# Optimization experiments

Hardware: AMD Instinct MI355X
Metric: run time of the kernel (lower is better)

The kernel has to match this reference:

```python
import jax, jax.numpy as jnp
import numpy as np

NUM_HEADS = 16
HIDDEN = 1024
HEAD_DIM = HIDDEN // NUM_HEADS


def setup_inputs() -> dict:
    key = jax.random.key(0)
    ks = jax.random.split(key, 8)
    B, S = 4, 1024
    scale = 0.02
    return {
        "hidden_states": jax.random.normal(ks[0], (B, S, HIDDEN), jnp.float32),
        "attention_mask": jnp.zeros((B, 1, 1, S), jnp.float32),
        "Wq": jax.random.normal(ks[1], (HIDDEN, HIDDEN), jnp.float32) * scale,
        "bq": jnp.zeros((HIDDEN,), jnp.float32),
        "Wk": jax.random.normal(ks[2], (HIDDEN, HIDDEN), jnp.float32) * scale,
        "bk": jnp.zeros((HIDDEN,), jnp.float32),
        "Wv": jax.random.normal(ks[3], (HIDDEN, HIDDEN), jnp.float32) * scale,
        "bv": jnp.zeros((HIDDEN,), jnp.float32),
    }


def _split_heads(x):
    # [B,S,H] -> [B,heads,S,head_dim]
    B, S, _ = x.shape
    return x.reshape(B, S, NUM_HEADS, HEAD_DIM).transpose(0, 2, 1, 3)


def reference(hidden_states, attention_mask, Wq, bq, Wk, bk, Wv, bv):
    # torch.nn.Linear convention: y = x @ W.T + b
    q = _split_heads(hidden_states @ Wq.T + bq)
    k = _split_heads(hidden_states @ Wk.T + bk)
    v = _split_heads(hidden_states @ Wv.T + bv)
    scores = jnp.einsum('bhqd,bhkd->bhqk', q, k) * (HEAD_DIM ** -0.5)
    scores = scores + attention_mask  # broadcast [B,1,1,S]
    probs = jax.nn.softmax(scores, axis=-1)
    context = jnp.einsum('bhqk,bhkd->bhqd', probs, v)  # [B,heads,S,head_dim]
    B, _, S, _ = context.shape
    return context.transpose(0, 2, 1, 3).reshape(B, S, HIDDEN)
```

## Files before the change

### kernel.cpp

```cpp
#include <hip/hip_runtime.h>
#include <hip/hip_bf16.h>
#include <stdint.h>

#define NH 16
#define HID 1024
#define HD 64
#define NB 4
#define SS 1024
#define MTOT (NB*SS)

typedef __attribute__((ext_vector_type(8))) short bf16x8;
typedef __attribute__((ext_vector_type(4))) float f32x4;
typedef __attribute__((ext_vector_type(16))) float f32x16;

#define LOG2E 1.44269504088896f

__device__ __forceinline__ unsigned short f2bf(float f) {
  union { float f; unsigned u; } v; v.f = f;
  unsigned u = v.u;
  return (unsigned short)((u + 0x7FFFu + ((u >> 16) & 1u)) >> 16);
}

__device__ __forceinline__ unsigned cvtpk(float lo, float hi) {
  unsigned r;
  asm("v_cvt_pk_bf16_f32 %0, %1, %2" : "=v"(r) : "v"(lo), "v"(hi));
  return r;
}

__device__ __forceinline__ void pl32swap(unsigned &a, unsigned &b) {
  asm("v_permlane32_swap_b32 %0, %1" : "+v"(a), "+v"(b));
}

__device__ __forceinline__ float exp2fast(float x) {
  float r;
  asm("v_exp_f32 %0, %1" : "=v"(r) : "v"(x));
  return r;
}

__device__ __forceinline__ void async16(void* lds, const void* g) {
  __builtin_amdgcn_global_load_lds(
      (const __attribute__((address_space(1))) unsigned*)g,
      (__attribute__((address_space(3))) unsigned*)lds, 16, 0, 0);
}

__global__ void cvt_all(const float4* __restrict__ X,
                        const float4* __restrict__ Wq,
                        const float4* __restrict__ Wk,
                        const float4* __restrict__ Wv,
                        ushort4* __restrict__ Xb,
                        ushort4* __restrict__ Wb) {
  int i = blockIdx.x * 256 + threadIdx.x;
  const float4* src; ushort4* dst; int idx;
  if (i < (MTOT * HID / 4)) {
    src = X; dst = Xb; idx = i;
  } else {
    int j = i - (MTOT * HID / 4);
    int sel = j >> 18;
    idx = j & 262143;
    src = (sel == 0) ? Wq : (sel == 1) ? Wk : Wv;
    dst = Wb + (size_t)sel * 262144;
  }
  float4 v = src[idx];
  ushort4 o;
  o.x = f2bf(v.x); o.y = f2bf(v.y); o.z = f2bf(v.z); o.w = f2bf(v.w);
  dst[idx] = o;
}

__global__ __launch_bounds__(256) void qkv_gemm(
    const ushort* __restrict__ Xb,
    const ushort* __restrict__ Wb,
    const float* __restrict__ bq,
    const float* __restrict__ bk,
    const float* __restrict__ bv,
    ushort* __restrict__ Q,
    ushort* __restrict__ K,
    ushort* __restrict__ Vt)
{
  __shared__ __attribute__((aligned(16))) ushort Al[3][128 * 32];
  __shared__ __attribute__((aligned(16))) ushort Bl[3][128 * 32];

  int bid = blockIdx.x;
  int swz = (bid & 7) * 96 + (bid >> 3);
  const int nbn = 3072 / 128;
  int bm = swz / nbn, bn = swz % nbn;
  int m0 = bm * 128, n0 = bn * 128;

  int tid = threadIdx.x;
  int wave = tid >> 6, lane = tid & 63;
  int g = lane >> 4, c = lane & 15;
  int wr = wave >> 1, wc = wave & 1;

  int srow = tid >> 2;
  int schunk = tid & 3;
  int ssw = (srow >> 1) & 3;
  const ushort* Asrc0 = Xb + (size_t)(m0 + srow) * 1024 + ((schunk ^ ssw) << 3);
  const ushort* Asrc1 = Xb + (size_t)(m0 + 64 + srow) * 1024 + ((schunk ^ ssw) << 3);
  const ushort* Bsrc0 = Wb + (size_t)(n0 + srow) * 1024 + ((schunk ^ ssw) << 3);
  const ushort* Bsrc1 = Wb + (size_t)(n0 + 64 + srow) * 1024 + ((schunk ^ ssw) << 3);
  int soff = srow * 64 + schunk * 16;

#define GSTAGE(bi) do {                                   \
    char* la_ = (char*)Al[bi]; char* lb_ = (char*)Bl[bi]; \
    async16(la_ + soff,        Asrc0);                    \
    async16(la_ + 4096 + soff, Asrc1);                    \
    async16(lb_ + soff,        Bsrc0);                    \
    async16(lb_ + 4096 + soff, Bsrc1);                    \
    Asrc0 += 32; Asrc1 += 32; Bsrc0 += 32; Bsrc1 += 32;   \
  } while (0)

  f32x4 acc[4][4] = {};
  int rsw = (c >> 1) & 3;
  int ch = ((g ^ rsw) << 4);

  GSTAGE(0);
  GSTAGE(1);

  int cur = 0, nxt = 2;
  for (int ks = 0; ks < 32; ++ks) {
    if (ks < 31) {
      asm volatile("s_waitcnt vmcnt(4)" ::: "memory");
    } else {
      asm volatile("s_waitcnt vmcnt(0)" ::: "memory");
    }
    __builtin_amdgcn_sched_barrier(0);
    __builtin_amdgcn_s_barrier();
    __builtin_amdgcn_sched_barrier(0);
    if (ks < 30) GSTAGE(nxt);

    const char* la = (const char*)Al[cur];
    const char* lb = (const char*)Bl[cur];
    bf16x8 a[4], b[4];
    #pragma unroll
    for (int m = 0; m < 4; ++m)
      a[m] = *(const bf16x8*)(la + (wr * 64 + m * 16 + c) * 64 + ch);
    #pragma unroll
    for (int n = 0; n < 4; ++n)
      b[n] = *(const bf16x8*)(lb + (wc * 64 + n * 16 + c) * 64 + ch);
    __builtin_amdgcn_s_setprio(1);
    #pragma unroll
    for (int m = 0; m < 4; ++m)
      #pragma unroll
      for (int n = 0; n < 4; ++n)
        acc[m][n] = __builtin_amdgcn_mfma_f32_16x16x32_bf16(a[m], b[n], acc[m][n], 0, 0, 0);
    __builtin_amdgcn_s_setprio(0);

    cur = (cur == 2) ? 0 : cur + 1;
    nxt = (nxt == 2) ? 0 : nxt + 1;
  }
#undef GSTAGE

  int sel = n0 >> 10;
  const float* bp = (sel == 0) ? bq : (sel == 1) ? bk : bv;
  float scl = (sel == 0) ? 0.125f * LOG2E : 1.0f;

  #pragma unroll
  for (int n = 0; n < 4; ++n) {
    int nn = (n0 & 1023) + wc * 64 + n * 16 + c;
    float bias = bp[nn];
    int h = nn >> 6, d = nn & 63;
    #pragma unroll
    for (int m = 0; m < 4; ++m) {
      int rowg = m0 + wr * 64 + m * 16 + g * 4;
      int bb = rowg >> 10;
      int s = rowg & 1023;
      #pragma unroll
      for (int r = 0; r < 4; ++r) {
        float val = (acc[m][n][r] + bias) * scl;
        unsigned short ob = f2bf(val);
        if (sel == 0)
          Q[(size_t)((bb * 16 + h) * 1024 + s + r) * 64 + d] = ob;
        else if (sel == 1)
          K[(size_t)((bb * 16 + h) * 1024 + s + r) * 64 + d] = ob;
        else
          Vt[(size_t)((bb * 16 + h) * 64 + d) * 1024 + s + r] = ob;
      }
    }
  }
}

__device__ __forceinline__ void build_pa(const f32x16& p, bf16x8& pa0, bf16x8& pa1) {
  unsigned W0 = cvtpk(p[0],  p[1]);
  unsigned W1 = cvtpk(p[2],  p[3]);
  unsigned W2 = cvtpk(p[4],  p[5]);
  unsigned W3 = cvtpk(p[6],  p[7]);
  unsigned W4 = cvtpk(p[8],  p[9]);
  unsigned W5 = cvtpk(p[10], p[11]);
  unsigned W6 = cvtpk(p[12], p[13]);
  unsigned W7 = cvtpk(p[14], p[15]);
  pl32swap(W0, W2);
  pl32swap(W1, W3);
  pl32swap(W4, W6);
  pl32swap(W5, W7);
  union { unsigned u[4]; bf16x8 v; } a0, a1;
  a0.u[0] = W0; a0.u[1] = W1; a0.u[2] = W2; a0.u[3] = W3;
  a1.u[0] = W4; a1.u[1] = W5; a1.u[2] = W6; a1.u[3] = W7;
  pa0 = a0.v; pa1 = a1.v;
}

__global__ __launch_bounds__(256) void attn(
    const ushort* __restrict__ Q,
    const ushort* __restrict__ K,
    const ushort* __restrict__ Vt,
    const float* __restrict__ mask,
    float* __restrict__ out)
{
  __shared__ __attribute__((aligned(16))) char kv_lds[3][16384];
  __shared__ float mask_s[SS];

  int blk = blockIdx.x;
  int xcd = blk & 7;
  int j = blk >> 3;
  int bh = xcd * 8 + (j >> 3);
  int qt = j & 7;
  int b = bh >> 4, h = bh & 15;
  int tid = threadIdx.x, wave = tid >> 6, lane = tid & 63;
  int r31 = lane & 31, hi = lane >> 5;
  int rsw = r31 & 7;
  int hib = hi << 4;
  int q0 = qt * 128 + wave * 32;

  const ushort* Qb = Q + (size_t)bh * SS * 64;
  const ushort* Kb = K + (size_t)bh * SS * 64;
  const ushort* Vb = Vt + (size_t)bh * 64 * SS;

  for (int i = tid; i < SS; i += 256) mask_s[i] = mask[b * SS + i] * LOG2E;

  bf16x8 qf[4];
  #pragma unroll
  for (int kp = 0; kp < 4; ++kp)
    qf[kp] = *(const bf16x8*)(Qb + (size_t)(q0 + r31) * 64 + kp * 16 + hi * 8);

  int srow = lane >> 3;
  int schunk = lane & 7;
  const ushort* sptr[4];
  int soff[4];
  #pragma unroll
  for (int j2 = 0; j2 < 4; ++j2) {
    soff[j2] = wave * 4096 + j2 * 1024;
    if (wave < 2) {
      int row = wave * 32 + j2 * 8 + srow;
      sptr[j2] = Kb + (size_t)row * 64 + ((schunk ^ srow) << 3);
    } else {
      int d = (wave - 2) * 32 + j2 * 8 + srow;
      sptr[j2] = Vb + (size_t)d * SS + ((schunk ^ srow) << 3);
    }
  }
  const int sstep = (wave < 2) ? 64 * 64 : 64;

#define STAGE(bufidx) do {                              \
    char* lb_ = kv_lds[bufidx];                         \
    async16(lb_ + soff[0], sptr[0]);                    \
    async16(lb_ + soff[1], sptr[1]);                    \
    async16(lb_ + soff[2], sptr[2]);                    \
    async16(lb_ + soff[3], sptr[3]);                    \
    sptr[0] += sstep; sptr[1] += sstep;                 \
    sptr[2] += sstep; sptr[3] += sstep;                 \
  } while (0)

  __syncthreads();
  STAGE(0);
  STAGE(1);

  f32x16 o0 = (f32x16)0.0f, o1 = (f32x16)0.0f;
  float mrow = 0.f, lrow = 0.f;

  int cur = 0, nxt = 2;
  for (int it = 0; it < 16; ++it) {
    if (it < 15) {
      asm volatile("s_waitcnt vmcnt(4)" ::: "memory");
    } else {
      asm volatile("s_waitcnt vmcnt(0)" ::: "memory");
    }
    __builtin_amdgcn_sched_barrier(0);
    __builtin_amdgcn_s_barrier();
    __builtin_amdgcn_sched_barrier(0);
    if (it < 14) STAGE(nxt);

    const char* kb0 = kv_lds[cur];
    const char* vb0 = kv_lds[cur] + 8192;

    f32x16 s0 = (f32x16)0.0f, s1 = (f32x16)0.0f;
    __builtin_amdgcn_s_setprio(1);
    #pragma unroll
    for (int kp = 0; kp < 4; ++kp) {
      int ch = (((kp << 1) | hi) ^ rsw) << 4;
      bf16x8 ka = *(const bf16x8*)(kb0 + r31 * 128 + ch);
      bf16x8 kc = *(const bf16x8*)(kb0 + (32 + r31) * 128 + ch);
      s0 = __builtin_amdgcn_mfma_f32_32x32x16_bf16(ka, qf[kp], s0, 0, 0, 0);
      s1 = __builtin_amdgcn_mfma_f32_32x32x16_bf16(kc, qf[kp], s1, 0, 0, 0);
    }
    __builtin_amdgcn_s_setprio(0);

    int kv = it * 64;
    #pragma unroll
    for (int sq = 0; sq < 4; ++sq) {
      f32x4 mk0 = *(const f32x4*)(&mask_s[kv + sq * 8 + hi * 4]);
      f32x4 mk1 = *(const f32x4*)(&mask_s[kv + 32 + sq * 8 + hi * 4]);
      #pragma unroll
      for (int r = 0; r < 4; ++r) {
        s0[sq * 4 + r] += mk0[r];
        s1[sq * 4 + r] += mk1[r];
      }
    }

    float mx = s0[0];
    #pragma unroll
    for (int i = 1; i < 16; ++i) mx = fmaxf(mx, s0[i]);
    #pragma unroll
    for (int i = 0; i < 16; ++i) mx = fmaxf(mx, s1[i]);
    mx = fmaxf(mx, __shfl_xor(mx, 32));

    if (!__all(mx <= mrow + 11.5416f)) {
      float mn = fmaxf(mrow, mx);
      float sc = exp2fast(mrow - mn);
      mrow = mn;
      lrow *= sc;
      #pragma unroll
      for (int i = 0; i < 16; ++i) {
        int qh = (i & 3) + 8 * (i >> 2);
        float scq = __uint_as_float((unsigned)__builtin_amdgcn_ds_bpermute(
            (qh << 2) + hib, (int)__float_as_uint(sc)));
        o0[i] *= scq; o1[i] *= scq;
      }
    }

    f32x16 p0, p1;
    float rs = 0.f;
    #pragma unroll
    for (int i = 0; i < 16; ++i) { float e = exp2fast(s0[i] - mrow); p0[i] = e; rs += e; }
    #pragma unroll
    for (int i = 0; i < 16; ++i) { float e = exp2fast(s1[i] - mrow); p1[i] = e; rs += e; }
    rs += __shfl_xor(rs, 32);
    lrow += rs;

    #pragma unroll
    for (int T = 0; T < 2; ++T) {
      bf16x8 pa0, pa1;
      build_pa(T ? p1 : p0, pa0, pa1);
      __builtin_amdgcn_s_setprio(1);
      #pragma unroll
      for (int kh = 0; kh < 2; ++kh) {
        int kap = 2 * T + kh;
        int ch = (((kap << 1) | hi) ^ rsw) << 4;
        bf16x8 va = *(const bf16x8*)(vb0 + r31 * 128 + ch);
        bf16x8 vc = *(const bf16x8*)(vb0 + (32 + r31) * 128 + ch);
        bf16x8 pf = kh ? pa1 : pa0;
        o0 = __builtin_amdgcn_mfma_f32_32x32x16_bf16(pf, va, o0, 0, 0, 0);
        o1 = __builtin_amdgcn_mfma_f32_32x32x16_bf16(pf, vc, o1, 0, 0, 0);
      }
      __builtin_amdgcn_s_setprio(0);
    }

    cur = (cur == 2) ? 0 : cur + 1;
    nxt = (nxt == 2) ? 0 : nxt + 1;
  }
#undef STAGE

  float inv = 1.0f / lrow;
  #pragma unroll
  for (int i = 0; i < 16; ++i) {
    int qh = (i & 3) + 8 * (i >> 2);
    float li = __uint_as_float((unsigned)__builtin_amdgcn_ds_bpermute(
        (qh << 2) + hib, (int)__float_as_uint(inv)));
    int row = q0 + qh + 4 * hi;
    float* op = out + (size_t)(b * SS + row) * 1024 + h * 64 + r31;
    op[0]  = o0[i] * li;
    op[32] = o1[i] * li;
  }
}

extern "C" void kernel_launch(void* const* d_in, const int* in_sizes, int n_in,
                              void* d_out, int out_size, void* d_ws, size_t ws_size,
                              hipStream_t stream) {
  const float* hs   = (const float*)d_in[0];
  const float* mask = (const float*)d_in[1];
  const float* Wq   = (const float*)d_in[2];
  const float* bq   = (const float*)d_in[3];
  const float* Wk   = (const float*)d_in[4];
  const float* bk   = (const float*)d_in[5];
  const float* Wv   = (const float*)d_in[6];
  const float* bv   = (const float*)d_in[7];
  float* out = (float*)d_out;

  char* ws = (char*)d_ws;
  ushort* Xb = (ushort*)(ws);
  ushort* Wb = (ushort*)(ws + (8u  << 20));
  ushort* Qp = (ushort*)(ws + (14u << 20));
  ushort* Kp = (ushort*)(ws + (22u << 20));
  ushort* Vt = (ushort*)(ws + (30u << 20));

  cvt_all<<<7168, 256, 0, stream>>>((const float4*)hs, (const float4*)Wq,
                                    (const float4*)Wk, (const float4*)Wv,
                                    (ushort4*)Xb, (ushort4*)Wb);
  qkv_gemm<<<768, 256, 0, stream>>>(Xb, Wb, bq, bk, bv, Qp, Kp, Vt);
  attn<<<512, 256, 0, stream>>>(Qp, Kp, Vt, mask, out);
}
```

Measured before the change: 85.83 us.

## Rewrite QKV GEMM with 256x256 tiles, 8 waves and ping-pong LDS schedule

Replaces the 128x128-tile, 4-wave triple-buffered QKV GEMM with a 256x256-tile, 512-thread kernel. It uses 64-wide K steps, 128KB of double-buffered LDS and an interleaved schedule that alternates sub-tile loads and MFMA groups between barriers. The aim is more data reuse per LDS byte and better overlap of global loads with MFMA. The trade-off is that only 192 blocks are launched, and with 128KB of LDS per block this can leave many CUs idle. The many extra barriers also add sync overhead.

```diff
diff --git a/kernel.cpp b/kernel.cpp
--- a/kernel.cpp
+++ b/kernel.cpp
@@ -66,7 +66,7 @@
   dst[idx] = o;
 }
 
-__global__ __launch_bounds__(256) void qkv_gemm(
+__global__ __launch_bounds__(512, 2) void qkv_gemm(
     const ushort* __restrict__ Xb,
     const ushort* __restrict__ Wb,
     const float* __restrict__ bq,
@@ -76,78 +76,129 @@
     ushort* __restrict__ K,
     ushort* __restrict__ Vt)
 {
-  __shared__ __attribute__((aligned(16))) ushort Al[3][128 * 32];
-  __shared__ __attribute__((aligned(16))) ushort Bl[3][128 * 32];
+  __shared__ __attribute__((aligned(16))) char lds_[131072];
+  char* ldsA = lds_;
+  char* ldsB = lds_ + 65536;
 
   int bid = blockIdx.x;
-  int swz = (bid & 7) * 96 + (bid >> 3);
-  const int nbn = 3072 / 128;
-  int bm = swz / nbn, bn = swz % nbn;
-  int m0 = bm * 128, n0 = bn * 128;
+  int swz = (bid & 7) * 24 + (bid >> 3);
+  int bm = swz / 12, bn = swz % 12;
+  int m0 = bm * 256, n0 = bn * 256;
 
   int tid = threadIdx.x;
   int wave = tid >> 6, lane = tid & 63;
   int g = lane >> 4, c = lane & 15;
-  int wr = wave >> 1, wc = wave & 1;
-
-  int srow = tid >> 2;
-  int schunk = tid & 3;
-  int ssw = (srow >> 1) & 3;
-  const ushort* Asrc0 = Xb + (size_t)(m0 + srow) * 1024 + ((schunk ^ ssw) << 3);
-  const ushort* Asrc1 = Xb + (size_t)(m0 + 64 + srow) * 1024 + ((schunk ^ ssw) << 3);
-  const ushort* Bsrc0 = Wb + (size_t)(n0 + srow) * 1024 + ((schunk ^ ssw) << 3);
-  const ushort* Bsrc1 = Wb + (size_t)(n0 + 64 + srow) * 1024 + ((schunk ^ ssw) << 3);
-  int soff = srow * 64 + schunk * 16;
-
-#define GSTAGE(bi) do {                                   \
-    char* la_ = (char*)Al[bi]; char* lb_ = (char*)Bl[bi]; \
-    async16(la_ + soff,        Asrc0);                    \
-    async16(la_ + 4096 + soff, Asrc1);                    \
-    async16(lb_ + soff,        Bsrc0);                    \
-    async16(lb_ + 4096 + soff, Bsrc1);                    \
-    Asrc0 += 32; Asrc1 += 32; Bsrc0 += 32; Bsrc1 += 32;   \
-  } while (0)
-
-  f32x4 acc[4][4] = {};
-  int rsw = (c >> 1) & 3;
-  int ch = ((g ^ rsw) << 4);
-
-  GSTAGE(0);
-  GSTAGE(1);
-
-  int cur = 0, nxt = 2;
-  for (int ks = 0; ks < 32; ++ks) {
-    if (ks < 31) {
-      asm volatile("s_waitcnt vmcnt(4)" ::: "memory");
-    } else {
-      asm volatile("s_waitcnt vmcnt(0)" ::: "memory");
-    }
-    __builtin_amdgcn_sched_barrier(0);
-    __builtin_amdgcn_s_barrier();
-    __builtin_amdgcn_sched_barrier(0);
-    if (ks < 30) GSTAGE(nxt);
-
-    const char* la = (const char*)Al[cur];
-    const char* lb = (const char*)Bl[cur];
-    bf16x8 a[4], b[4];
-    #pragma unroll
-    for (int m = 0; m < 4; ++m)
-      a[m] = *(const bf16x8*)(la + (wr * 64 + m * 16 + c) * 64 + ch);
-    #pragma unroll
-    for (int n = 0; n < 4; ++n)
-      b[n] = *(const bf16x8*)(lb + (wc * 64 + n * 16 + c) * 64 + ch);
-    __builtin_amdgcn_s_setprio(1);
-    #pragma unroll
-    for (int m = 0; m < 4; ++m)
-      #pragma unroll
-      for (int n = 0; n < 4; ++n)
-        acc[m][n] = __builtin_amdgcn_mfma_f32_16x16x32_bf16(a[m], b[n], acc[m][n], 0, 0, 0);
-    __builtin_amdgcn_s_setprio(0);
-
-    cur = (cur == 2) ? 0 : cur + 1;
-    nxt = (nxt == 2) ? 0 : nxt + 1;
-  }
-#undef GSTAGE
+  int wr = wave >> 2, wc = wave & 3;
+
+  int r0 = tid >> 3, ck = tid & 7;
+  int gck = ck ^ (r0 & 7);
+  const ushort* As0 = Xb + (size_t)(m0 + r0) * 1024 + gck * 8;
+  const ushort* As1 = As0 + 128 * 1024;
+  const ushort* Bs0 = Wb + (size_t)(n0 + r0) * 1024 + gck * 8;
+  const ushort* Bs1 = Bs0 + 128 * 1024;
+  int sdst = tid * 16;
+
+#define STG_A(d, h, t) do { \
+    const ushort* _s = ((h) ? As1 : As0) + (t) * 64; \
+    char* _d = ldsA + ((d) * 2 + (h)) * 16384 + sdst; \
+    async16(_d, _s); async16(_d + 8192, _s + 64 * 1024); } while (0)
+#define STG_B(d, h, t) do { \
+    const ushort* _s = ((h) ? Bs1 : Bs0) + (t) * 64; \
+    char* _d = ldsB + ((d) * 2 + (h)) * 16384 + sdst; \
+    async16(_d, _s); async16(_d + 8192, _s + 64 * 1024); } while (0)
+
+  int ch0 = (g ^ (c & 7)) << 4;
+  int ch1 = ((4 + g) ^ (c & 7)) << 4;
+
+  bf16x8 a[4][2], b[2][2], b2[2][2];
+  f32x4 acc[8][4] = {};
+
+#define LDA_(mlo, d) do { \
+    const char* _p = ldsA + ((d) * 2 + wr) * 16384; \
+    _Pragma("unroll") \
+    for (int mm = 0; mm < 4; ++mm) { \
+      int _ro = ((mlo) * 64 + mm * 16 + c) * 128; \
+      a[mm][0] = *(const bf16x8*)(_p + _ro + ch0); \
+      a[mm][1] = *(const bf16x8*)(_p + _ro + ch1); } } while (0)
+#define LDB_(dst, nlo, d) do { \
+    const char* _p = ldsB + ((d) * 2 + (wc >> 1)) * 16384 + ((wc & 1) * 64) * 128; \
+    _Pragma("unroll") \
+    for (int nn2 = 0; nn2 < 2; ++nn2) { \
+      int _ro = (((nlo) * 2 + nn2) * 16 + c) * 128; \
+      dst[nn2][0] = *(const bf16x8*)(_p + _ro + ch0); \
+      dst[nn2][1] = *(const bf16x8*)(_p + _ro + ch1); } } while (0)
+
+#define BARRIER() do { __builtin_amdgcn_sched_barrier(0); \
+    __builtin_amdgcn_s_barrier(); __builtin_amdgcn_sched_barrier(0); } while (0)
+
+#define MF_(mlo, bf, nlo) do { \
+    __builtin_amdgcn_s_setprio(1); \
+    _Pragma("unroll") \
+    for (int mm = 0; mm < 4; ++mm) \
+      _Pragma("unroll") \
+      for (int nn2 = 0; nn2 < 2; ++nn2) { \
+        acc[(mlo)*4+mm][(nlo)*2+nn2] = __builtin_amdgcn_mfma_f32_16x16x32_bf16( \
+            a[mm][0], bf[nn2][0], acc[(mlo)*4+mm][(nlo)*2+nn2], 0, 0, 0); \
+        acc[(mlo)*4+mm][(nlo)*2+nn2] = __builtin_amdgcn_mfma_f32_16x16x32_bf16( \
+            a[mm][1], bf[nn2][1], acc[(mlo)*4+mm][(nlo)*2+nn2], 0, 0, 0); } \
+    __builtin_amdgcn_s_setprio(0); } while (0)
+
+  STG_B(0, 0, 0); STG_B(0, 1, 0);
+  STG_A(0, 0, 0); STG_A(0, 1, 0);
+  STG_B(1, 0, 1); STG_B(1, 1, 1);
+  asm volatile("s_waitcnt vmcnt(4)" ::: "memory");
+  BARRIER();
+
+  for (int i2 = 0; i2 < 8; ++i2) {
+    int t1 = 2 * i2 + 1, t2 = 2 * i2 + 2, t3 = 2 * i2 + 3;
+    LDA_(0, 0); LDB_(b, 0, 0);
+    STG_A(1, 0, t1);
+    BARRIER();
+    MF_(0, b, 0);
+    BARRIER();
+    LDB_(b2, 1, 0);
+    STG_A(1, 1, t1);
+    BARRIER();
+    MF_(0, b2, 1);
+    BARRIER();
+    LDA_(1, 0);
+    STG_B(0, 0, t2);
+    BARRIER();
+    MF_(1, b, 0);
+    BARRIER();
+    STG_B(0, 1, t2);
+    asm volatile("s_waitcnt vmcnt(4)" ::: "memory");
+    BARRIER();
+    MF_(1, b2, 1);
+    BARRIER();
+    LDA_(0, 1); LDB_(b, 0, 1);
+    STG_A(0, 0, t2);
+    BARRIER();
+    MF_(0, b, 0);
+    BARRIER();
+    LDB_(b2, 1, 1);
+    STG_A(0, 1, t2);
+    BARRIER();
+    MF_(0, b2, 1);
+    BARRIER();
+    LDA_(1, 1);
+    STG_B(1, 0, t3);
+    BARRIER();
+    MF_(1, b, 0);
+    BARRIER();
+    STG_B(1, 1, t3);
+    asm volatile("s_waitcnt vmcnt(4)" ::: "memory");
+    BARRIER();
+    MF_(1, b2, 1);
+    BARRIER();
+  }
+  asm volatile("s_waitcnt vmcnt(0)" ::: "memory");
+#undef STG_A
+#undef STG_B
+#undef LDA_
+#undef LDB_
+#undef MF_
+#undef BARRIER
 
   int sel = n0 >> 10;
   const float* bp = (sel == 0) ? bq : (sel == 1) ? bk : bv;
@@ -159,8 +210,8 @@
     float bias = bp[nn];
     int h = nn >> 6, d = nn & 63;
     #pragma unroll
-    for (int m = 0; m < 4; ++m) {
-      int rowg = m0 + wr * 64 + m * 16 + g * 4;
+    for (int m = 0; m < 8; ++m) {
+      int rowg = m0 + wr * 128 + m * 16 + g * 4;
       int bb = rowg >> 10;
       int s = rowg & 1023;
       #pragma unroll
@@ -392,6 +443,6 @@
   cvt_all<<<7168, 256, 0, stream>>>((const float4*)hs, (const float4*)Wq,
                                     (const float4*)Wk, (const float4*)Wv,
                                     (ushort4*)Xb, (ushort4*)Wb);
-  qkv_gemm<<<768, 256, 0, stream>>>(Xb, Wb, bq, bk, bv, Qp, Kp, Vt);
+  qkv_gemm<<<192, 512, 0, stream>>>(Xb, Wb, bq, bk, bv, Qp, Kp, Vt);
   attn<<<512, 256, 0, stream>>>(Qp, Kp, Vt, mask, out);
 }
```

After: 98.89 us. +15.2%, slower.

## Retile QKV GEMM to 128x64 blocks with two waves and double buffering

Applied to the files above, without the earlier changes.

The QKV projection GEMM moves from 128x128 tiles with four waves and a 3-stage LDS ring to 128x64 tiles with two waves and a 2-stage double buffer, launching twice as many blocks. Each block issues its next-stage loads before waiting and adds a second barrier per k-step to protect buffer reuse. The aim is more blocks in flight across the CUs to fill the machine better on a 768-block grid. In exchange, B-tile reuse per block drops, each wave loads more A data, and pipelining depth shrinks.

```diff
diff --git a/kernel.cpp b/kernel.cpp
--- a/kernel.cpp
+++ b/kernel.cpp
@@ -66,7 +66,7 @@
   dst[idx] = o;
 }
 
-__global__ __launch_bounds__(256) void qkv_gemm(
+__global__ __launch_bounds__(128) void qkv_gemm(
     const ushort* __restrict__ Xb,
     const ushort* __restrict__ Wb,
     const float* __restrict__ bq,
@@ -76,36 +76,41 @@
     ushort* __restrict__ K,
     ushort* __restrict__ Vt)
 {
-  __shared__ __attribute__((aligned(16))) ushort Al[3][128 * 32];
-  __shared__ __attribute__((aligned(16))) ushort Bl[3][128 * 32];
+  __shared__ __attribute__((aligned(16))) ushort Al[2][128 * 32];
+  __shared__ __attribute__((aligned(16))) ushort Bl[2][64 * 32];
 
   int bid = blockIdx.x;
-  int swz = (bid & 7) * 96 + (bid >> 3);
-  const int nbn = 3072 / 128;
-  int bm = swz / nbn, bn = swz % nbn;
-  int m0 = bm * 128, n0 = bn * 128;
+  int swz = (bid & 7) * 192 + (bid >> 3);
+  int bm = swz / 48, bn = swz % 48;
+  int m0 = bm * 128, n0 = bn * 64;
 
   int tid = threadIdx.x;
   int wave = tid >> 6, lane = tid & 63;
   int g = lane >> 4, c = lane & 15;
-  int wr = wave >> 1, wc = wave & 1;
-
-  int srow = tid >> 2;
-  int schunk = tid & 3;
-  int ssw = (srow >> 1) & 3;
-  const ushort* Asrc0 = Xb + (size_t)(m0 + srow) * 1024 + ((schunk ^ ssw) << 3);
-  const ushort* Asrc1 = Xb + (size_t)(m0 + 64 + srow) * 1024 + ((schunk ^ ssw) << 3);
-  const ushort* Bsrc0 = Wb + (size_t)(n0 + srow) * 1024 + ((schunk ^ ssw) << 3);
-  const ushort* Bsrc1 = Wb + (size_t)(n0 + 64 + srow) * 1024 + ((schunk ^ ssw) << 3);
-  int soff = srow * 64 + schunk * 16;
+
+  int r0 = tid >> 2;
+  int ck = tid & 3;
+  int gck = ck ^ ((r0 >> 1) & 3);
+  const ushort* As[4];
+  const ushort* Bs[2];
+  #pragma unroll
+  for (int i = 0; i < 4; ++i)
+    As[i] = Xb + (size_t)(m0 + r0 + 32 * i) * 1024 + gck * 8;
+  #pragma unroll
+  for (int i = 0; i < 2; ++i)
+    Bs[i] = Wb + (size_t)(n0 + r0 + 32 * i) * 1024 + gck * 8;
+  int sdst = tid * 16;
 
 #define GSTAGE(bi) do {                                   \
     char* la_ = (char*)Al[bi]; char* lb_ = (char*)Bl[bi]; \
-    async16(la_ + soff,        Asrc0);                    \
-    async16(la_ + 4096 + soff, Asrc1);                    \
-    async16(lb_ + soff,        Bsrc0);                    \
-    async16(lb_ + 4096 + soff, Bsrc1);                    \
-    Asrc0 += 32; Asrc1 += 32; Bsrc0 += 32; Bsrc1 += 32;   \
+    async16(la_ + sdst,        As[0]);                    \
+    async16(la_ + 2048 + sdst, As[1]);                    \
+    async16(la_ + 4096 + sdst, As[2]);                    \
+    async16(la_ + 6144 + sdst, As[3]);                    \
+    async16(lb_ + sdst,        Bs[0]);                    \
+    async16(lb_ + 2048 + sdst, Bs[1]);                    \
+    As[0] += 32; As[1] += 32; As[2] += 32; As[3] += 32;   \
+    Bs[0] += 32; Bs[1] += 32;                             \
   } while (0)
 
   f32x4 acc[4][4] = {};
@@ -113,29 +118,28 @@
   int ch = ((g ^ rsw) << 4);
 
   GSTAGE(0);
-  GSTAGE(1);
-
-  int cur = 0, nxt = 2;
+
+  int cur = 0;
   for (int ks = 0; ks < 32; ++ks) {
     if (ks < 31) {
-      asm volatile("s_waitcnt vmcnt(4)" ::: "memory");
+      GSTAGE(cur ^ 1);
+      asm volatile("s_waitcnt vmcnt(6)" ::: "memory");
     } else {
       asm volatile("s_waitcnt vmcnt(0)" ::: "memory");
     }
     __builtin_amdgcn_sched_barrier(0);
     __builtin_amdgcn_s_barrier();
     __builtin_amdgcn_sched_barrier(0);
-    if (ks < 30) GSTAGE(nxt);
 
     const char* la = (const char*)Al[cur];
     const char* lb = (const char*)Bl[cur];
     bf16x8 a[4], b[4];
     #pragma unroll
     for (int m = 0; m < 4; ++m)
-      a[m] = *(const bf16x8*)(la + (wr * 64 + m * 16 + c) * 64 + ch);
+      a[m] = *(const bf16x8*)(la + (wave * 64 + m * 16 + c) * 64 + ch);
     #pragma unroll
     for (int n = 0; n < 4; ++n)
-      b[n] = *(const bf16x8*)(lb + (wc * 64 + n * 16 + c) * 64 + ch);
+      b[n] = *(const bf16x8*)(lb + (n * 16 + c) * 64 + ch);
     __builtin_amdgcn_s_setprio(1);
     #pragma unroll
     for (int m = 0; m < 4; ++m)
@@ -144,23 +148,24 @@
         acc[m][n] = __builtin_amdgcn_mfma_f32_16x16x32_bf16(a[m], b[n], acc[m][n], 0, 0, 0);
     __builtin_amdgcn_s_setprio(0);
 
-    cur = (cur == 2) ? 0 : cur + 1;
-    nxt = (nxt == 2) ? 0 : nxt + 1;
+    __builtin_amdgcn_sched_barrier(0);
+    __builtin_amdgcn_s_barrier();
+    cur ^= 1;
   }
 #undef GSTAGE
 
   int sel = n0 >> 10;
   const float* bp = (sel == 0) ? bq : (sel == 1) ? bk : bv;
   float scl = (sel == 0) ? 0.125f * LOG2E : 1.0f;
+  int h = (n0 & 1023) >> 6;
 
   #pragma unroll
   for (int n = 0; n < 4; ++n) {
-    int nn = (n0 & 1023) + wc * 64 + n * 16 + c;
-    float bias = bp[nn];
-    int h = nn >> 6, d = nn & 63;
+    int d = n * 16 + c;
+    float bias = bp[(n0 & 1023) + d];
     #pragma unroll
     for (int m = 0; m < 4; ++m) {
-      int rowg = m0 + wr * 64 + m * 16 + g * 4;
+      int rowg = m0 + wave * 64 + m * 16 + g * 4;
       int bb = rowg >> 10;
       int s = rowg & 1023;
       #pragma unroll
@@ -392,6 +397,6 @@
   cvt_all<<<7168, 256, 0, stream>>>((const float4*)hs, (const float4*)Wq,
                                     (const float4*)Wk, (const float4*)Wv,
                                     (ushort4*)Xb, (ushort4*)Wb);
-  qkv_gemm<<<768, 256, 0, stream>>>(Xb, Wb, bq, bk, bv, Qp, Kp, Vt);
+  qkv_gemm<<<1536, 128, 0, stream>>>(Xb, Wb, bq, bk, bv, Qp, Kp, Vt);
   attn<<<512, 256, 0, stream>>>(Qp, Kp, Vt, mask, out);
 }
```

Result: slower. 93.10 us (+8.5%).

## Load GEMM B and attention V operands directly into registers, bypassing LDS

Applied to the files above, without the earlier changes.

In the QKV GEMM, the W tile is no longer staged through shared memory. Each wave loads its B fragments straight from global memory into double-buffered registers, while X still goes through the LDS ring. The block-to-tile mapping is also changed so each XCD owns a fixed set of M rows, and an occupancy hint is added. In the attention kernel, V fragments are read from global memory into registers each iteration and only K stays in the LDS triple buffer. This cuts LDS use and ds_read traffic, but the direct-to-register global loads are less coalesced and raise register pressure.

```diff
diff --git a/kernel.cpp b/kernel.cpp
--- a/kernel.cpp
+++ b/kernel.cpp
@@ -66,7 +66,7 @@
   dst[idx] = o;
 }
 
-__global__ __launch_bounds__(256) void qkv_gemm(
+__global__ __launch_bounds__(256, 3) void qkv_gemm(
     const ushort* __restrict__ Xb,
     const ushort* __restrict__ Wb,
     const float* __restrict__ bq,
@@ -77,12 +77,12 @@
     ushort* __restrict__ Vt)
 {
   __shared__ __attribute__((aligned(16))) ushort Al[3][128 * 32];
-  __shared__ __attribute__((aligned(16))) ushort Bl[3][128 * 32];
 
   int bid = blockIdx.x;
-  int swz = (bid & 7) * 96 + (bid >> 3);
-  const int nbn = 3072 / 128;
-  int bm = swz / nbn, bn = swz % nbn;
+  int xcd = bid & 7;
+  int j = bid >> 3;
+  int bm = 4 * xcd + (j & 3);
+  int bn = j >> 2;
   int m0 = bm * 128, n0 = bn * 128;
 
   int tid = threadIdx.x;
@@ -90,64 +90,73 @@
   int g = lane >> 4, c = lane & 15;
   int wr = wave >> 1, wc = wave & 1;
 
-  int srow = tid >> 2;
-  int schunk = tid & 3;
+  int srow = tid >> 2, schunk = tid & 3;
   int ssw = (srow >> 1) & 3;
-  const ushort* Asrc0 = Xb + (size_t)(m0 + srow) * 1024 + ((schunk ^ ssw) << 3);
-  const ushort* Asrc1 = Xb + (size_t)(m0 + 64 + srow) * 1024 + ((schunk ^ ssw) << 3);
-  const ushort* Bsrc0 = Wb + (size_t)(n0 + srow) * 1024 + ((schunk ^ ssw) << 3);
-  const ushort* Bsrc1 = Wb + (size_t)(n0 + 64 + srow) * 1024 + ((schunk ^ ssw) << 3);
+  const ushort* As0 = Xb + (size_t)(m0 + srow) * 1024 + ((schunk ^ ssw) << 3);
+  const ushort* As1 = As0 + (size_t)64 * 1024;
   int soff = srow * 64 + schunk * 16;
 
-#define GSTAGE(bi) do {                                   \
-    char* la_ = (char*)Al[bi]; char* lb_ = (char*)Bl[bi]; \
-    async16(la_ + soff,        Asrc0);                    \
-    async16(la_ + 4096 + soff, Asrc1);                    \
-    async16(lb_ + soff,        Bsrc0);                    \
-    async16(lb_ + 4096 + soff, Bsrc1);                    \
-    Asrc0 += 32; Asrc1 += 32; Bsrc0 += 32; Bsrc1 += 32;   \
-  } while (0)
+  const ushort* Bg = Wb + (size_t)(n0 + wc * 64 + c) * 1024 + g * 8;
+
+#define STAGE_A(bi, kk) do { \
+    char* la_ = (char*)Al[bi]; \
+    async16(la_ + soff,        As0 + (kk) * 32); \
+    async16(la_ + 4096 + soff, As1 + (kk) * 32); } while (0)
+
+#define LOADB(dst, kk) do { \
+    _Pragma("unroll") \
+    for (int n = 0; n < 4; ++n) \
+      dst[n] = *(const bf16x8*)(Bg + (size_t)n * 16384 + (kk) * 32); } while (0)
 
   f32x4 acc[4][4] = {};
   int rsw = (c >> 1) & 3;
   int ch = ((g ^ rsw) << 4);
 
-  GSTAGE(0);
-  GSTAGE(1);
+  bf16x8 b0[4], b1[4];
+  STAGE_A(0, 0);
+  STAGE_A(1, 1);
+  LOADB(b0, 0);
+  __syncthreads();
+
+#define GSTEP(KS, CURBUF, STGBUF, BUSE, BLOAD) do {                       \
+    __builtin_amdgcn_sched_barrier(0);                                    \
+    __builtin_amdgcn_s_barrier();                                         \
+    __builtin_amdgcn_sched_barrier(0);                                    \
+    int kst_ = (KS) + 2 < 32 ? (KS) + 2 : 31;                             \
+    int kld_ = (KS) + 1 < 32 ? (KS) + 1 : 31;                             \
+    STAGE_A(STGBUF, kst_);                                                \
+    LOADB(BLOAD, kld_);                                                   \
+    const char* la_ = (const char*)Al[CURBUF];                            \
+    bf16x8 a_[4];                                                         \
+    _Pragma("unroll")                                                     \
+    for (int m = 0; m < 4; ++m)                                           \
+      a_[m] = *(const bf16x8*)(la_ + (wr * 64 + m * 16 + c) * 64 + ch);   \
+    asm volatile("s_waitcnt vmcnt(6)" ::: "memory");                      \
+    __builtin_amdgcn_sched_barrier(0);                                    \
+    __builtin_amdgcn_s_setprio(1);                                        \
+    _Pragma("unroll")                                                     \
+    for (int m = 0; m < 4; ++m)                                           \
+      _Pragma("unroll")                                                   \
+      for (int n = 0; n < 4; ++n)                                         \
+        acc[m][n] = __builtin_amdgcn_mfma_f32_16x16x32_bf16(              \
+            a_[m], BUSE[n], acc[m][n], 0, 0, 0);                          \
+    __builtin_amdgcn_s_setprio(0);                                        \
+  } while (0)
 
   int cur = 0, nxt = 2;
-  for (int ks = 0; ks < 32; ++ks) {
-    if (ks < 31) {
-      asm volatile("s_waitcnt vmcnt(4)" ::: "memory");
-    } else {
-      asm volatile("s_waitcnt vmcnt(0)" ::: "memory");
-    }
-    __builtin_amdgcn_sched_barrier(0);
-    __builtin_amdgcn_s_barrier();
-    __builtin_amdgcn_sched_barrier(0);
-    if (ks < 30) GSTAGE(nxt);
-
-    const char* la = (const char*)Al[cur];
-    const char* lb = (const char*)Bl[cur];
-    bf16x8 a[4], b[4];
-    #pragma unroll
-    for (int m = 0; m < 4; ++m)
-      a[m] = *(const bf16x8*)(la + (wr * 64 + m * 16 + c) * 64 + ch);
-    #pragma unroll
-    for (int n = 0; n < 4; ++n)
-      b[n] = *(const bf16x8*)(lb + (wc * 64 + n * 16 + c) * 64 + ch);
-    __builtin_amdgcn_s_setprio(1);
-    #pragma unroll
-    for (int m = 0; m < 4; ++m)
-      #pragma unroll
-      for (int n = 0; n < 4; ++n)
-        acc[m][n] = __builtin_amdgcn_mfma_f32_16x16x32_bf16(a[m], b[n], acc[m][n], 0, 0, 0);
-    __builtin_amdgcn_s_setprio(0);
-
+  #pragma unroll 1
+  for (int ks = 0; ks < 32; ks += 2) {
+    GSTEP(ks, cur, nxt, b0, b1);
     cur = (cur == 2) ? 0 : cur + 1;
     nxt = (nxt == 2) ? 0 : nxt + 1;
-  }
-#undef GSTAGE
+    GSTEP(ks + 1, cur, nxt, b1, b0);
+    cur = (cur == 2) ? 0 : cur + 1;
+    nxt = (nxt == 2) ? 0 : nxt + 1;
+  }
+  asm volatile("s_waitcnt vmcnt(0)" ::: "memory");
+#undef GSTEP
+#undef STAGE_A
+#undef LOADB
 
   int sel = n0 >> 10;
   const float* bp = (sel == 0) ? bq : (sel == 1) ? bk : bv;
@@ -197,14 +206,14 @@
   pa0 = a0.v; pa1 = a1.v;
 }
 
-__global__ __launch_bounds__(256) void attn(
+__global__ __launch_bounds__(256, 2) void attn(
     const ushort* __restrict__ Q,
     const ushort* __restrict__ K,
     const ushort* __restrict__ Vt,
     const float* __restrict__ mask,
     float* __restrict__ out)
 {
-  __shared__ __attribute__((aligned(16))) char kv_lds[3][16384];
+  __shared__ __attribute__((aligned(16))) char k_lds[3][8192];
   __shared__ float mask_s[SS];
 
   int blk = blockIdx.x;
@@ -230,55 +239,45 @@
   for (int kp = 0; kp < 4; ++kp)
     qf[kp] = *(const bf16x8*)(Qb + (size_t)(q0 + r31) * 64 + kp * 16 + hi * 8);
 
-  int srow = lane >> 3;
-  int schunk = lane & 7;
-  const ushort* sptr[4];
-  int soff[4];
-  #pragma unroll
-  for (int j2 = 0; j2 < 4; ++j2) {
-    soff[j2] = wave * 4096 + j2 * 1024;
-    if (wave < 2) {
-      int row = wave * 32 + j2 * 8 + srow;
-      sptr[j2] = Kb + (size_t)row * 64 + ((schunk ^ srow) << 3);
-    } else {
-      int d = (wave - 2) * 32 + j2 * 8 + srow;
-      sptr[j2] = Vb + (size_t)d * SS + ((schunk ^ srow) << 3);
-    }
-  }
-  const int sstep = (wave < 2) ? 64 * 64 : 64;
-
-#define STAGE(bufidx) do {                              \
-    char* lb_ = kv_lds[bufidx];                         \
-    async16(lb_ + soff[0], sptr[0]);                    \
-    async16(lb_ + soff[1], sptr[1]);                    \
-    async16(lb_ + soff[2], sptr[2]);                    \
-    async16(lb_ + soff[3], sptr[3]);                    \
-    sptr[0] += sstep; sptr[1] += sstep;                 \
-    sptr[2] += sstep; sptr[3] += sstep;                 \
-  } while (0)
-
+  int krow = tid >> 3;
+  int gck = (tid & 7) ^ (krow & 7);
+  const ushort* Ks0 = Kb + (size_t)krow * 64 + gck * 8;
+  const ushort* Ks1 = Kb + (size_t)(krow + 32) * 64 + gck * 8;
+  int soff = tid * 16;
+
+#define STAGE_K(bi, t64) do { \
+    char* lb_ = k_lds[bi]; \
+    async16(lb_ + soff,        Ks0 + (size_t)(t64) * 4096); \
+    async16(lb_ + 4096 + soff, Ks1 + (size_t)(t64) * 4096); } while (0)
+
+  const ushort* Vg0 = Vb + (size_t)r31 * SS + hi * 8;
+  const ushort* Vg1 = Vb + (size_t)(32 + r31) * SS + hi * 8;
+
+  STAGE_K(0, 0);
+  STAGE_K(1, 1);
   __syncthreads();
-  STAGE(0);
-  STAGE(1);
 
   f32x16 o0 = (f32x16)0.0f, o1 = (f32x16)0.0f;
   float mrow = 0.f, lrow = 0.f;
 
   int cur = 0, nxt = 2;
+  #pragma unroll 1
   for (int it = 0; it < 16; ++it) {
-    if (it < 15) {
-      asm volatile("s_waitcnt vmcnt(4)" ::: "memory");
-    } else {
-      asm volatile("s_waitcnt vmcnt(0)" ::: "memory");
-    }
     __builtin_amdgcn_sched_barrier(0);
     __builtin_amdgcn_s_barrier();
     __builtin_amdgcn_sched_barrier(0);
-    if (it < 14) STAGE(nxt);
-
-    const char* kb0 = kv_lds[cur];
-    const char* vb0 = kv_lds[cur] + 8192;
-
+
+    int kv = it * 64;
+    bf16x8 vA[4], vC[4];
+    #pragma unroll
+    for (int kap = 0; kap < 4; ++kap) {
+      vA[kap] = *(const bf16x8*)(Vg0 + kv + kap * 16);
+      vC[kap] = *(const bf16x8*)(Vg1 + kv + kap * 16);
+    }
+    int kst = it + 2 < 16 ? it + 2 : 15;
+    STAGE_K(nxt, kst);
+
+    const char* kb0 = k_lds[cur];
     f32x16 s0 = (f32x16)0.0f, s1 = (f32x16)0.0f;
     __builtin_amdgcn_s_setprio(1);
     #pragma unroll
@@ -291,7 +290,6 @@
     }
     __builtin_amdgcn_s_setprio(0);
 
-    int kv = it * 64;
     #pragma unroll
     for (int sq = 0; sq < 4; ++sq) {
       f32x4 mk0 = *(const f32x4*)(&mask_s[kv + sq * 8 + hi * 4]);
@@ -333,6 +331,9 @@
     rs += __shfl_xor(rs, 32);
     lrow += rs;
 
+    asm volatile("s_waitcnt vmcnt(2)" ::: "memory");
+    __builtin_amdgcn_sched_barrier(0);
+
     #pragma unroll
     for (int T = 0; T < 2; ++T) {
       bf16x8 pa0, pa1;
@@ -341,12 +342,9 @@
       #pragma unroll
       for (int kh = 0; kh < 2; ++kh) {
         int kap = 2 * T + kh;
-        int ch = (((kap << 1) | hi) ^ rsw) << 4;
-        bf16x8 va = *(const bf16x8*)(vb0 + r31 * 128 + ch);
-        bf16x8 vc = *(const bf16x8*)(vb0 + (32 + r31) * 128 + ch);
         bf16x8 pf = kh ? pa1 : pa0;
-        o0 = __builtin_amdgcn_mfma_f32_32x32x16_bf16(pf, va, o0, 0, 0, 0);
-        o1 = __builtin_amdgcn_mfma_f32_32x32x16_bf16(pf, vc, o1, 0, 0, 0);
+        o0 = __builtin_amdgcn_mfma_f32_32x32x16_bf16(pf, vA[kap], o0, 0, 0, 0);
+        o1 = __builtin_amdgcn_mfma_f32_32x32x16_bf16(pf, vC[kap], o1, 0, 0, 0);
       }
       __builtin_amdgcn_s_setprio(0);
     }
@@ -354,7 +352,8 @@
     cur = (cur == 2) ? 0 : cur + 1;
     nxt = (nxt == 2) ? 0 : nxt + 1;
   }
-#undef STAGE
+#undef STAGE_K
+  asm volatile("s_waitcnt vmcnt(0)" ::: "memory");
 
   float inv = 1.0f / lrow;
   #pragma unroll
```

New measurement: 116.5 us. +35.7%, slower.
